# Kernel tuning notes

Measured on AMD Instinct MI355X. Metric: run time of the kernel, lower is better.

## Reference

```python
import jax, jax.numpy as jnp
import numpy as np

D_MODEL = 1024
NUM_HEADS = 16
D_HEAD = D_MODEL // NUM_HEADS
THETA = 10000.0


def setup_inputs() -> dict:
    key = jax.random.key(0)
    ks = jax.random.split(key, 5)
    B, S = 2, 2048
    std = np.sqrt(2.0 / (D_MODEL + D_MODEL))
    return {
        "x": jax.random.normal(ks[0], (B, S, D_MODEL), dtype=jnp.float32),
        "token_positions": jnp.arange(S, dtype=jnp.int32),
        "wq": jax.random.normal(ks[1], (D_MODEL, D_MODEL), dtype=jnp.float32) * std,
        "wk": jax.random.normal(ks[2], (D_MODEL, D_MODEL), dtype=jnp.float32) * std,
        "wv": jax.random.normal(ks[3], (D_MODEL, D_MODEL), dtype=jnp.float32) * std,
        "wo": jax.random.normal(ks[4], (D_MODEL, D_MODEL), dtype=jnp.float32) * std,
    }


def _rope(x, token_positions):
    # x: [B, H, S, D_HEAD]; token_positions: [S]
    freq_idx = jnp.arange(0, D_HEAD, 2, dtype=jnp.float32)
    inv_freq = THETA ** (-freq_idx / D_HEAD)                      # [D_HEAD/2]
    angles = token_positions.astype(jnp.float32)[:, None] * inv_freq  # [S, D_HEAD/2]
    cos = jnp.cos(angles)[None, None, :, :]
    sin = jnp.sin(angles)[None, None, :, :]
    x_even = x[..., 0::2]
    x_odd = x[..., 1::2]
    rot_even = x_even * cos - x_odd * sin
    rot_odd = x_even * sin + x_odd * cos
    # interleave pairs back: [..., pairs, 2] -> [..., D_HEAD]
    return jnp.stack((rot_even, rot_odd), axis=-1).reshape(x.shape)


def reference(x, token_positions, wq, wk, wv, wo):
    B, S, _ = x.shape
    def proj(w):
        y = jnp.einsum('bsi,oi->bso', x, w)
        return y.reshape(B, S, NUM_HEADS, D_HEAD).transpose(0, 2, 1, 3)  # [B,H,S,Dh]
    q = _rope(proj(wq), token_positions)
    k = _rope(proj(wk), token_positions)
    v = proj(wv)
    scores = jnp.einsum('bhqd,bhkd->bhqk', q, k) / jnp.sqrt(jnp.float32(D_HEAD))
    causal = jnp.tril(jnp.ones((S, S), dtype=bool))
    scores = jnp.where(causal, scores, -jnp.inf)
    probs = jax.nn.softmax(scores, axis=-1)
    attn = jnp.einsum('bhqk,bhkd->bhqd', probs, v)
    attn = attn.transpose(0, 2, 1, 3).reshape(B, S, D_MODEL)
    return jnp.einsum('bsi,oi->bso', attn, wo)
```

## Files before the change

kernel.cpp:

```cpp
#include <hip/hip_runtime.h>
#include <math.h>

#define D_MODEL 1024
#define NUM_HEADS 16
#define D_HEAD 64
#define SEQ 2048
#define BATCH 2

typedef __attribute__((ext_vector_type(8))) short short8;
typedef __attribute__((ext_vector_type(4))) short short4v;
typedef __attribute__((ext_vector_type(4))) float float4v;
typedef __attribute__((ext_vector_type(2))) unsigned int uint2v;

__device__ __forceinline__ short f2bf(float f) {
    unsigned u = __float_as_uint(f);
    u += 0x7FFFu + ((u >> 16) & 1u);
    return (short)(u >> 16);
}

__device__ __forceinline__ float fexp2(float x) {
    return __builtin_amdgcn_exp2f(x);
}

__global__ __launch_bounds__(256) void cvt_bf16_kernel(
    const float* __restrict__ x,  const float* __restrict__ wq,
    const float* __restrict__ wk, const float* __restrict__ wv,
    const float* __restrict__ wo, const int* __restrict__ pos,
    short* __restrict__ xb,  short* __restrict__ wqb,
    short* __restrict__ wkb, short* __restrict__ wvb,
    short* __restrict__ wob,
    float* __restrict__ costab, float* __restrict__ sintab)
{
    const int a = blockIdx.y;
    if (a == 5) {
        const int idx = blockIdx.x * 256 + threadIdx.x;
        if (idx < SEQ * 32) {
            const int s = idx >> 5, fi = idx & 31;
            const float p = (float)pos[s];
            const float inv_freq = exp2f((float)fi * -0.4152410118609203f);
            float sn, cs;
            sincosf(p * inv_freq, &sn, &cs);
            costab[idx] = cs;
            sintab[idx] = sn;
        }
        return;
    }
    const float* src = (a == 0) ? x : (a == 1) ? wq : (a == 2) ? wk : (a == 3) ? wv : wo;
    short* dst = (a == 0) ? xb : (a == 1) ? wqb : (a == 2) ? wkb : (a == 3) ? wvb : wob;
    const int n = (a == 0) ? (BATCH * SEQ * D_MODEL) : (D_MODEL * D_MODEL);
    const int i = (blockIdx.x * 256 + threadIdx.x) * 8;
    if (i >= n) return;
    const float4 v0 = *(const float4*)(src + i);
    const float4 v1 = *(const float4*)(src + i + 4);
    short8 r;
    r[0] = f2bf(v0.x); r[1] = f2bf(v0.y); r[2] = f2bf(v0.z); r[3] = f2bf(v0.w);
    r[4] = f2bf(v1.x); r[5] = f2bf(v1.y); r[6] = f2bf(v1.z); r[7] = f2bf(v1.w);
    *(short8*)(dst + i) = r;
}

__device__ __forceinline__ void gemm_core_db(
    const short* __restrict__ a, const short* __restrict__ b,
    short* smem, int m0, int n0, float4v acc[4][4], const int nk)
{
    const int tid = threadIdx.x;
    const int lane = tid & 63;
    const int l15 = lane & 15, quad = lane >> 4;
    const int wave = tid >> 6;
    const int mw = (wave & 1) * 64, nw = (wave >> 1) * 64;
    const int srow = tid >> 2;
    const int scol = (tid & 3) * 8;
    const int ssw = (((tid & 3) ^ ((srow >> 1) & 3))) * 8;
    const int xsw = (l15 >> 1) & 3;

    const short* ag = a + (size_t)(m0 + srow) * D_MODEL + scol;
    const short* bg = b + (size_t)(n0 + srow) * D_MODEL + scol;

    short* bufA[2] = { smem,        smem + 8192 };
    short* bufB[2] = { smem + 4096, smem + 12288 };

    short8 ga0 = *(const short8*)(ag);
    short8 ga1 = *(const short8*)(ag + (size_t)64 * D_MODEL);
    short8 gb0 = *(const short8*)(bg);
    short8 gb1 = *(const short8*)(bg + (size_t)64 * D_MODEL);
    *(short8*)&bufA[0][srow * 32 + ssw]        = ga0;
    *(short8*)&bufA[0][(64 + srow) * 32 + ssw] = ga1;
    *(short8*)&bufB[0][srow * 32 + ssw]        = gb0;
    *(short8*)&bufB[0][(64 + srow) * 32 + ssw] = gb1;
    ga0 = *(const short8*)(ag + 32);
    ga1 = *(const short8*)(ag + 32 + (size_t)64 * D_MODEL);
    gb0 = *(const short8*)(bg + 32);
    gb1 = *(const short8*)(bg + 32 + (size_t)64 * D_MODEL);

    for (int k = 0; k < nk; k++) {
        __syncthreads();
        if (k + 1 < nk) {
            short* bA = bufA[(k + 1) & 1];
            short* bB = bufB[(k + 1) & 1];
            *(short8*)&bA[srow * 32 + ssw]        = ga0;
            *(short8*)&bA[(64 + srow) * 32 + ssw] = ga1;
            *(short8*)&bB[srow * 32 + ssw]        = gb0;
            *(short8*)&bB[(64 + srow) * 32 + ssw] = gb1;
        }
        if (k + 2 < nk) {
            const int off = (k + 2) * 32;
            ga0 = *(const short8*)(ag + off);
            ga1 = *(const short8*)(ag + off + (size_t)64 * D_MODEL);
            gb0 = *(const short8*)(bg + off);
            gb1 = *(const short8*)(bg + off + (size_t)64 * D_MODEL);
        }
        const short* lA = bufA[k & 1];
        const short* lB = bufB[k & 1];
        short8 af[4], bf[4];
        #pragma unroll
        for (int i = 0; i < 4; i++)
            af[i] = *(const short8*)&lA[(mw + i * 16 + l15) * 32 + (quad ^ xsw) * 8];
        #pragma unroll
        for (int i = 0; i < 4; i++)
            bf[i] = *(const short8*)&lB[(nw + i * 16 + l15) * 32 + (quad ^ xsw) * 8];
        #pragma unroll
        for (int mi = 0; mi < 4; mi++)
            #pragma unroll
            for (int ni = 0; ni < 4; ni++)
                acc[mi][ni] = __builtin_amdgcn_mfma_f32_16x16x32_bf16(
                    af[mi], bf[ni], acc[mi][ni], 0, 0, 0);
    }
}

__device__ __forceinline__ void gemm_core_out(
    const short* __restrict__ a, const short* __restrict__ b,
    short* smem, int m0, int n0, float4v acc[2][4])
{
    const int tid = threadIdx.x;
    const int lane = tid & 63;
    const int l15 = lane & 15, quad = lane >> 4;
    const int wave = tid >> 6;
    const int mw = wave * 32;
    const int srow = tid >> 2;
    const int scol = (tid & 3) * 8;
    const int ssw = (((tid & 3) ^ ((srow >> 1) & 3))) * 8;
    const int xsw = (l15 >> 1) & 3;

    const short* ag = a + (size_t)(m0 + srow) * D_MODEL + scol;
    const short* bg = b + (size_t)(n0 + srow) * D_MODEL + scol;

    short* bufA[2] = { smem,        smem + 6144 };
    short* bufB[2] = { smem + 4096, smem + 10240 };

    short8 ga0 = *(const short8*)(ag);
    short8 ga1 = *(const short8*)(ag + (size_t)64 * D_MODEL);
    short8 gb0 = *(const short8*)(bg);
    *(short8*)&bufA[0][srow * 32 + ssw]        = ga0;
    *(short8*)&bufA[0][(64 + srow) * 32 + ssw] = ga1;
    *(short8*)&bufB[0][srow * 32 + ssw]        = gb0;
    ga0 = *(const short8*)(ag + 32);
    ga1 = *(const short8*)(ag + 32 + (size_t)64 * D_MODEL);
    gb0 = *(const short8*)(bg + 32);

    for (int k = 0; k < 32; k++) {
        __syncthreads();
        if (k + 1 < 32) {
            short* bA = bufA[(k + 1) & 1];
            short* bB = bufB[(k + 1) & 1];
            *(short8*)&bA[srow * 32 + ssw]        = ga0;
            *(short8*)&bA[(64 + srow) * 32 + ssw] = ga1;
            *(short8*)&bB[srow * 32 + ssw]        = gb0;
        }
        if (k + 2 < 32) {
            const int off = (k + 2) * 32;
            ga0 = *(const short8*)(ag + off);
            ga1 = *(const short8*)(ag + off + (size_t)64 * D_MODEL);
            gb0 = *(const short8*)(bg + off);
        }
        const short* lA = bufA[k & 1];
        const short* lB = bufB[k & 1];
        short8 af[2], bf[4];
        #pragma unroll
        for (int i = 0; i < 2; i++)
            af[i] = *(const short8*)&lA[(mw + i * 16 + l15) * 32 + (quad ^ xsw) * 8];
        #pragma unroll
        for (int i = 0; i < 4; i++)
            bf[i] = *(const short8*)&lB[(i * 16 + l15) * 32 + (quad ^ xsw) * 8];
        #pragma unroll
        for (int mi = 0; mi < 2; mi++)
            #pragma unroll
            for (int ni = 0; ni < 4; ni++)
                acc[mi][ni] = __builtin_amdgcn_mfma_f32_16x16x32_bf16(
                    af[mi], bf[ni], acc[mi][ni], 0, 0, 0);
    }
}

__global__ __launch_bounds__(256) void qkv_mfma_kernel(
    const short* __restrict__ xb, const short* __restrict__ wqb,
    const short* __restrict__ wkb, const short* __restrict__ wvb,
    const float* __restrict__ costab, const float* __restrict__ sintab,
    short* __restrict__ Qb, short* __restrict__ Kb, short* __restrict__ Vt)
{
    __shared__ __align__(16) short smem[128 * 136];

    const int z = blockIdx.x >> 8;
    const int bid = blockIdx.x & 255;
    const int m0 = (bid & 31) * 128;
    const int n0 = (bid >> 5) * 128;
    const short* w = (z == 0) ? wqb : (z == 1) ? wkb : wvb;

    float4v acc[4][4];
    #pragma unroll
    for (int i = 0; i < 4; i++)
        #pragma unroll
        for (int j = 0; j < 4; j++)
            acc[i][j] = (float4v){0.f, 0.f, 0.f, 0.f};

    gemm_core_db(xb, w, smem, m0, n0, acc, 32);

    const int tid = threadIdx.x;
    const int lane = tid & 63;
    const int l15 = lane & 15, quad = lane >> 4;
    const int wave = tid >> 6;
    const int mw = (wave & 1) * 64, nw = (wave >> 1) * 64;
    const int s_base = m0 & (SEQ - 1);
    const int bb = m0 >> 11;

    __syncthreads();

    if (z == 2) {
        #pragma unroll
        for (int ni = 0; ni < 4; ni++) {
            #pragma unroll
            for (int mi = 0; mi < 4; mi++) {
                #pragma unroll
                for (int r = 0; r < 4; r++)
                    smem[(nw + ni * 16 + l15) * 136 + mw + mi * 16 + quad * 4 + r] =
                        f2bf(acc[mi][ni][r]);
            }
        }
        __syncthreads();
        #pragma unroll
        for (int it = 0; it < 8; it++) {
            const int nloc = it * 16 + (tid >> 4);
            const int mloc = (tid & 15) * 8;
            const short8 val = *(const short8*)&smem[nloc * 136 + mloc];
            const int n = n0 + nloc;
            const int h = n >> 6, d = n & 63;
            *(short8*)(Vt + ((size_t)(bb * NUM_HEADS + h) * D_HEAD + d) * SEQ +
                       s_base + mloc) = val;
        }
    } else {
        short* dst = (z == 0) ? Qb : Kb;
        const float qs = (z == 0) ? 0.18033688011112042f : 1.0f;
        #pragma unroll
        for (int ni = 0; ni < 4; ni++) {
            const int n = n0 + nw + ni * 16 + l15;
            const int d = n & 63;
            const int fi = d >> 1;
            #pragma unroll
            for (int mi = 0; mi < 4; mi++) {
                #pragma unroll
                for (int r = 0; r < 4; r++) {
                    const int mloc = mw + mi * 16 + quad * 4 + r;
                    const int ti = ((s_base + mloc) << 5) + fi;
                    const float cs = costab[ti];
                    const float sn = sintab[ti];
                    const float val = acc[mi][ni][r];
                    const float partner = __shfl_xor(val, 1, 64);
                    const float res = (l15 & 1) ? fmaf(partner, sn, val * cs)
                                                : fmaf(val, cs, -partner * sn);
                    smem[mloc * 136 + nw + ni * 16 + l15] = f2bf(res * qs);
                }
            }
        }
        __syncthreads();
        #pragma unroll
        for (int it = 0; it < 8; it++) {
            const int ri = it * 32 + (tid >> 3);
            const int mloc = ri & 127;
            const int hh = ri >> 7;
            const int nloc = hh * 64 + (tid & 7) * 8;
            const short8 val = *(const short8*)&smem[mloc * 136 + nloc];
            const int n = n0 + nloc;
            const int h = n >> 6, d = n & 63;
            *(short8*)(dst + ((size_t)(bb * NUM_HEADS + h) * SEQ + s_base + mloc) *
                       D_HEAD + d) = val;
        }
    }
}

__global__ __launch_bounds__(256) void attn_mfma_kernel(
    const short* __restrict__ Qb, const short* __restrict__ Kb,
    const short* __restrict__ Vt, short* __restrict__ Ab)
{
    __shared__ __align__(16) short lKa[64 * 32];
    __shared__ __align__(16) short lKb[64 * 32];
    __shared__ __align__(16) short lVa[64 * 32];
    __shared__ __align__(16) short lVb[64 * 32];
    __shared__ __align__(16) short lP[4][2][16 * 32];

    const int tid = threadIdx.x;
    const int lane = tid & 63;
    const int wave = tid >> 6;
    const int l15 = lane & 15;
    const int quad = lane >> 4;

    const int bh = blockIdx.x & (BATCH * NUM_HEADS - 1);
    const int qt = (SEQ / 64 - 1) - (blockIdx.x >> 5);
    const int q0w = qt * 64 + wave * 16;
    const int qcmp = q0w + l15;

    const short* Kg = Kb + (size_t)bh * SEQ * D_HEAD;
    const short* Vg = Vt + (size_t)bh * D_HEAD * SEQ;

    const short* Qrow = Qb + ((size_t)bh * SEQ + q0w + l15) * D_HEAD;
    const short8 qf0 = *(const short8*)(Qrow + quad * 8);
    const short8 qf1 = *(const short8*)(Qrow + 32 + quad * 8);

    float4v o0 = {0.f, 0.f, 0.f, 0.f}, o1 = o0, o2 = o0, o3 = o0;
    float lpA = 0.f, lpB = 0.f;

    const int nt = qt + 1;
    const int srow = tid >> 2;
    const int c4  = tid & 3;
    const int sch = c4 * 8;
    const int swoff = srow * 32 + ((c4 ^ ((srow >> 1) & 3)) * 8);
    const int xsw = (l15 >> 1) & 3;

    short8 k0 = *(const short8*)(Kg + (size_t)srow * D_HEAD + sch);
    short8 k1 = *(const short8*)(Kg + (size_t)srow * D_HEAD + sch + 32);
    short8 v0 = *(const short8*)(Vg + (size_t)srow * SEQ + sch);
    short8 v1 = *(const short8*)(Vg + (size_t)srow * SEQ + sch + 32);

#define ATTN_TILE_COMPUTE(KT0, MASKED)                                        \
    {                                                                         \
        short* PwA = &lP[wave][0][0];                                         \
        short* PwB = &lP[wave][1][0];                                         \
        _Pragma("unroll")                                                     \
        for (int g = 0; g < 4; g++) {                                         \
            float4v s = {0.f, 0.f, 0.f, 0.f};                                 \
            const int krow = (g * 16 + l15) * 32 + (quad ^ xsw) * 8;          \
            const short8 ka = *(const short8*)&lKa[krow];                     \
            const short8 kb = *(const short8*)&lKb[krow];                     \
            __builtin_amdgcn_s_setprio(1);                                    \
            s = __builtin_amdgcn_mfma_f32_16x16x32_bf16(ka, qf0, s, 0, 0, 0); \
            s = __builtin_amdgcn_mfma_f32_16x16x32_bf16(kb, qf1, s, 0, 0, 0); \
            __builtin_amdgcn_s_setprio(0);                                    \
            float e0, e1, e2, e3;                                             \
            if (MASKED) {                                                     \
                const int kbase = (KT0) + g * 16 + quad * 4;                  \
                e0 = (kbase + 0 <= qcmp) ? fexp2(s[0]) : 0.f;                 \
                e1 = (kbase + 1 <= qcmp) ? fexp2(s[1]) : 0.f;                 \
                e2 = (kbase + 2 <= qcmp) ? fexp2(s[2]) : 0.f;                 \
                e3 = (kbase + 3 <= qcmp) ? fexp2(s[3]) : 0.f;                 \
            } else {                                                          \
                e0 = fexp2(s[0]); e1 = fexp2(s[1]);                           \
                e2 = fexp2(s[2]); e3 = fexp2(s[3]);                           \
            }                                                                 \
            lpA += e0 + e2;                                                   \
            lpB += e1 + e3;                                                   \
            unsigned int pw0, pw1;                                            \
            asm("v_cvt_pk_bf16_f32 %0, %1, %2" : "=v"(pw0) : "v"(e0), "v"(e1)); \
            asm("v_cvt_pk_bf16_f32 %0, %1, %2" : "=v"(pw1) : "v"(e2), "v"(e3)); \
            uint2v pk; pk[0] = pw0; pk[1] = pw1;                              \
            short* Pd = (g < 2) ? PwA : PwB;                                  \
            const int ps = ((((g & 1) * 2 + (quad >> 1)) ^ xsw) * 8) +        \
                           (quad & 1) * 4;                                    \
            *(uint2v*)&Pd[l15 * 32 + ps] = pk;                                \
        }                                                                     \
        const int prow = l15 * 32 + (quad ^ xsw) * 8;                         \
        const short8 pa0 = *(const short8*)&PwA[prow];                        \
        const short8 pa1 = *(const short8*)&PwB[prow];                        \
        __builtin_amdgcn_s_setprio(1);                                        \
        _Pragma("unroll")                                                     \
        for (int j = 0; j < 4; j++) {                                         \
            const int vrow = (j * 16 + l15) * 32 + (quad ^ xsw) * 8;          \
            const short8 va = *(const short8*)&lVa[vrow];                     \
            const short8 vb = *(const short8*)&lVb[vrow];                     \
            float4v* oj = (j == 0) ? &o0 : (j == 1) ? &o1 : (j == 2) ? &o2 : &o3;       \
            *oj = __builtin_amdgcn_mfma_f32_16x16x32_bf16(pa0, va, *oj, 0, 0, 0);       \
            *oj = __builtin_amdgcn_mfma_f32_16x16x32_bf16(pa1, vb, *oj, 0, 0, 0);       \
        }                                                                     \
        __builtin_amdgcn_s_setprio(0);                                        \
    }

    for (int t = 0; t < nt - 1; t++) {
        const int kt0 = t * 64;
        __syncthreads();
        *(short8*)&lKa[swoff] = k0;
        *(short8*)&lKb[swoff] = k1;
        *(short8*)&lVa[swoff] = v0;
        *(short8*)&lVb[swoff] = v1;
        __syncthreads();
        k0 = *(const short8*)(Kg + (size_t)(kt0 + 64 + srow) * D_HEAD + sch);
        k1 = *(const short8*)(Kg + (size_t)(kt0 + 64 + srow) * D_HEAD + sch + 32);
        v0 = *(const short8*)(Vg + (size_t)srow * SEQ + kt0 + 64 + sch);
        v1 = *(const short8*)(Vg + (size_t)srow * SEQ + kt0 + 64 + sch + 32);
        ATTN_TILE_COMPUTE(kt0, false)
    }
    {
        const int kt0 = (nt - 1) * 64;
        __syncthreads();
        *(short8*)&lKa[swoff] = k0;
        *(short8*)&lKb[swoff] = k1;
        *(short8*)&lVa[swoff] = v0;
        *(short8*)&lVb[swoff] = v1;
        __syncthreads();
        ATTN_TILE_COMPUTE(kt0, true)
    }
#undef ATTN_TILE_COMPUTE

    float lp = lpA + lpB;
    lp += __shfl_xor(lp, 16, 64);
    lp += __shfl_xor(lp, 32, 64);

    const int b = bh >> 4, h = bh & 15;
    short* Ap = Ab + ((size_t)(b * SEQ) + q0w + quad * 4) * D_MODEL + h * D_HEAD;
    #pragma unroll
    for (int r = 0; r < 4; r++) {
        const float inv = 1.0f / __shfl(lp, quad * 4 + r, 64);
        Ap[(size_t)r * D_MODEL + l15]      = f2bf(o0[r] * inv);
        Ap[(size_t)r * D_MODEL + 16 + l15] = f2bf(o1[r] * inv);
        Ap[(size_t)r * D_MODEL + 32 + l15] = f2bf(o2[r] * inv);
        Ap[(size_t)r * D_MODEL + 48 + l15] = f2bf(o3[r] * inv);
    }
}

__global__ __launch_bounds__(256) void out_mfma_kernel(
    const short* __restrict__ Ab, const short* __restrict__ wob,
    float* __restrict__ out)
{
    __shared__ __align__(16) short smem[12288];

    const int bid = blockIdx.x;
    const int m0 = (bid & 31) * 128;
    const int n0 = (bid >> 5) * 64;

    float4v acc[2][4];
    #pragma unroll
    for (int i = 0; i < 2; i++)
        #pragma unroll
        for (int j = 0; j < 4; j++)
            acc[i][j] = (float4v){0.f, 0.f, 0.f, 0.f};

    gemm_core_out(Ab, wob, smem, m0, n0, acc);

    const int tid = threadIdx.x;
    const int lane = tid & 63;
    const int l15 = lane & 15, quad = lane >> 4;
    const int wave = tid >> 6;
    const int mw = wave * 32;

    #pragma unroll
    for (int mi = 0; mi < 2; mi++) {
        #pragma unroll
        for (int r = 0; r < 4; r++) {
            const int m = m0 + mw + mi * 16 + quad * 4 + r;
            float* op = out + (size_t)m * D_MODEL + n0 + l15;
            #pragma unroll
            for (int ni = 0; ni < 4; ni++)
                op[ni * 16] = acc[mi][ni][r];
        }
    }
}

extern "C" void kernel_launch(void* const* d_in, const int* in_sizes, int n_in,
                              void* d_out, int out_size, void* d_ws, size_t ws_size,
                              hipStream_t stream)
{
    const float* x  = (const float*)d_in[0];
    const int*  pos = (const int*)d_in[1];
    const float* wq = (const float*)d_in[2];
    const float* wk = (const float*)d_in[3];
    const float* wv = (const float*)d_in[4];
    const float* wo = (const float*)d_in[5];
    float* out = (float*)d_out;

    const size_t nx = (size_t)BATCH * SEQ * D_MODEL;
    const size_t nw = (size_t)D_MODEL * D_MODEL;
    short* xb  = (short*)d_ws;
    short* wqb = xb + nx;
    short* wkb = wqb + nw;
    short* wvb = wkb + nw;
    short* wob = wvb + nw;
    short* Qb  = wob + nw;
    short* Kb  = Qb + nx;
    short* Vt  = Kb + nx;
    short* Ab  = Vt + nx;
    float* costab = (float*)(Ab + nx);
    float* sintab = costab + SEQ * 32;

    dim3 blk(256);
    cvt_bf16_kernel<<<dim3(2048, 6), blk, 0, stream>>>(x, wq, wk, wv, wo, pos,
                                                       xb, wqb, wkb, wvb, wob,
                                                       costab, sintab);
    qkv_mfma_kernel<<<dim3(768), blk, 0, stream>>>(xb, wqb, wkb, wvb,
                                                   costab, sintab, Qb, Kb, Vt);
    attn_mfma_kernel<<<dim3(BATCH * NUM_HEADS * (SEQ / 64)), blk, 0, stream>>>(Qb, Kb, Vt, Ab);
    out_mfma_kernel<<<dim3(512), blk, 0, stream>>>(Ab, wob, out);
}
```

Before: 174.7 us.

## Fuse fp32-to-bf16 conversion into GEMM loaders and compute RoPE inline

Removes the separate conversion kernel. The QKV and output GEMMs now load fp32 inputs and weights directly and convert them to bf16 with packed cvt instructions while staging into shared memory. RoPE sin and cos are computed in the epilogue with hardware sin/cos on fractional revolutions instead of reading precomputed tables. This saves one launch and the bf16 round-trip through global memory, at the cost of twice the global bytes per GEMM tile load, redundant conversion of x across the column blocks, and lower-precision hardware trig.

Measured after the change: 208.2 us. 1.19x slower.

```diff
diff --git a/kernel.cpp b/kernel.cpp
--- a/kernel.cpp
+++ b/kernel.cpp
@@ -8,9 +8,9 @@
 #define BATCH 2
 
 typedef __attribute__((ext_vector_type(8))) short short8;
-typedef __attribute__((ext_vector_type(4))) short short4v;
 typedef __attribute__((ext_vector_type(4))) float float4v;
 typedef __attribute__((ext_vector_type(2))) unsigned int uint2v;
+typedef __attribute__((ext_vector_type(4))) unsigned int uint4v;
 
 __device__ __forceinline__ short f2bf(float f) {
     unsigned u = __float_as_uint(f);
@@ -22,45 +22,25 @@
     return __builtin_amdgcn_exp2f(x);
 }
 
-__global__ __launch_bounds__(256) void cvt_bf16_kernel(
-    const float* __restrict__ x,  const float* __restrict__ wq,
-    const float* __restrict__ wk, const float* __restrict__ wv,
-    const float* __restrict__ wo, const int* __restrict__ pos,
-    short* __restrict__ xb,  short* __restrict__ wqb,
-    short* __restrict__ wkb, short* __restrict__ wvb,
-    short* __restrict__ wob,
-    float* __restrict__ costab, float* __restrict__ sintab)
-{
-    const int a = blockIdx.y;
-    if (a == 5) {
-        const int idx = blockIdx.x * 256 + threadIdx.x;
-        if (idx < SEQ * 32) {
-            const int s = idx >> 5, fi = idx & 31;
-            const float p = (float)pos[s];
-            const float inv_freq = exp2f((float)fi * -0.4152410118609203f);
-            float sn, cs;
-            sincosf(p * inv_freq, &sn, &cs);
-            costab[idx] = cs;
-            sintab[idx] = sn;
-        }
-        return;
-    }
-    const float* src = (a == 0) ? x : (a == 1) ? wq : (a == 2) ? wk : (a == 3) ? wv : wo;
-    short* dst = (a == 0) ? xb : (a == 1) ? wqb : (a == 2) ? wkb : (a == 3) ? wvb : wob;
-    const int n = (a == 0) ? (BATCH * SEQ * D_MODEL) : (D_MODEL * D_MODEL);
-    const int i = (blockIdx.x * 256 + threadIdx.x) * 8;
-    if (i >= n) return;
-    const float4 v0 = *(const float4*)(src + i);
-    const float4 v1 = *(const float4*)(src + i + 4);
-    short8 r;
-    r[0] = f2bf(v0.x); r[1] = f2bf(v0.y); r[2] = f2bf(v0.z); r[3] = f2bf(v0.w);
-    r[4] = f2bf(v1.x); r[5] = f2bf(v1.y); r[6] = f2bf(v1.z); r[7] = f2bf(v1.w);
-    *(short8*)(dst + i) = r;
-}
-
-__device__ __forceinline__ void gemm_core_db(
-    const short* __restrict__ a, const short* __restrict__ b,
-    short* smem, int m0, int n0, float4v acc[4][4], const int nk)
+__device__ __forceinline__ uint4v cvt8(float4 lo, float4 hi) {
+    uint4v r;
+    asm("v_cvt_pk_bf16_f32 %0, %1, %2" : "=v"(r[0]) : "v"(lo.x), "v"(lo.y));
+    asm("v_cvt_pk_bf16_f32 %0, %1, %2" : "=v"(r[1]) : "v"(lo.z), "v"(lo.w));
+    asm("v_cvt_pk_bf16_f32 %0, %1, %2" : "=v"(r[2]) : "v"(hi.x), "v"(hi.y));
+    asm("v_cvt_pk_bf16_f32 %0, %1, %2" : "=v"(r[3]) : "v"(hi.z), "v"(hi.w));
+    return r;
+}
+
+__device__ __forceinline__ void sincos_rev(float rev, float* sn, float* cs) {
+    float fr;
+    asm("v_fract_f32 %0, %1" : "=v"(fr) : "v"(rev));
+    asm("v_sin_f32 %0, %1" : "=v"(*sn) : "v"(fr));
+    asm("v_cos_f32 %0, %1" : "=v"(*cs) : "v"(fr));
+}
+
+__device__ __forceinline__ void gemm_core_f32(
+    const float* __restrict__ a, const float* __restrict__ b,
+    short* smem, int m0, int n0, float4v acc[4][4])
 {
     const int tid = threadIdx.x;
     const int lane = tid & 63;
@@ -72,41 +52,53 @@
     const int ssw = (((tid & 3) ^ ((srow >> 1) & 3))) * 8;
     const int xsw = (l15 >> 1) & 3;
 
-    const short* ag = a + (size_t)(m0 + srow) * D_MODEL + scol;
-    const short* bg = b + (size_t)(n0 + srow) * D_MODEL + scol;
+    const float* ag = a + (size_t)(m0 + srow) * D_MODEL + scol;
+    const float* bg = b + (size_t)(n0 + srow) * D_MODEL + scol;
 
     short* bufA[2] = { smem,        smem + 8192 };
     short* bufB[2] = { smem + 4096, smem + 12288 };
 
-    short8 ga0 = *(const short8*)(ag);
-    short8 ga1 = *(const short8*)(ag + (size_t)64 * D_MODEL);
-    short8 gb0 = *(const short8*)(bg);
-    short8 gb1 = *(const short8*)(bg + (size_t)64 * D_MODEL);
-    *(short8*)&bufA[0][srow * 32 + ssw]        = ga0;
-    *(short8*)&bufA[0][(64 + srow) * 32 + ssw] = ga1;
-    *(short8*)&bufB[0][srow * 32 + ssw]        = gb0;
-    *(short8*)&bufB[0][(64 + srow) * 32 + ssw] = gb1;
-    ga0 = *(const short8*)(ag + 32);
-    ga1 = *(const short8*)(ag + 32 + (size_t)64 * D_MODEL);
-    gb0 = *(const short8*)(bg + 32);
-    gb1 = *(const short8*)(bg + 32 + (size_t)64 * D_MODEL);
-
-    for (int k = 0; k < nk; k++) {
-        __syncthreads();
-        if (k + 1 < nk) {
+    float4 a0l = *(const float4*)(ag);
+    float4 a0h = *(const float4*)(ag + 4);
+    float4 a1l = *(const float4*)(ag + (size_t)64 * D_MODEL);
+    float4 a1h = *(const float4*)(ag + (size_t)64 * D_MODEL + 4);
+    float4 b0l = *(const float4*)(bg);
+    float4 b0h = *(const float4*)(bg + 4);
+    float4 b1l = *(const float4*)(bg + (size_t)64 * D_MODEL);
+    float4 b1h = *(const float4*)(bg + (size_t)64 * D_MODEL + 4);
+    *(uint4v*)&bufA[0][srow * 32 + ssw]        = cvt8(a0l, a0h);
+    *(uint4v*)&bufA[0][(64 + srow) * 32 + ssw] = cvt8(a1l, a1h);
+    *(uint4v*)&bufB[0][srow * 32 + ssw]        = cvt8(b0l, b0h);
+    *(uint4v*)&bufB[0][(64 + srow) * 32 + ssw] = cvt8(b1l, b1h);
+    a0l = *(const float4*)(ag + 32);
+    a0h = *(const float4*)(ag + 36);
+    a1l = *(const float4*)(ag + 32 + (size_t)64 * D_MODEL);
+    a1h = *(const float4*)(ag + 36 + (size_t)64 * D_MODEL);
+    b0l = *(const float4*)(bg + 32);
+    b0h = *(const float4*)(bg + 36);
+    b1l = *(const float4*)(bg + 32 + (size_t)64 * D_MODEL);
+    b1h = *(const float4*)(bg + 36 + (size_t)64 * D_MODEL);
+
+    for (int k = 0; k < 32; k++) {
+        __syncthreads();
+        if (k + 1 < 32) {
             short* bA = bufA[(k + 1) & 1];
             short* bB = bufB[(k + 1) & 1];
-            *(short8*)&bA[srow * 32 + ssw]        = ga0;
-            *(short8*)&bA[(64 + srow) * 32 + ssw] = ga1;
-            *(short8*)&bB[srow * 32 + ssw]        = gb0;
-            *(short8*)&bB[(64 + srow) * 32 + ssw] = gb1;
-        }
-        if (k + 2 < nk) {
+            *(uint4v*)&bA[srow * 32 + ssw]        = cvt8(a0l, a0h);
+            *(uint4v*)&bA[(64 + srow) * 32 + ssw] = cvt8(a1l, a1h);
+            *(uint4v*)&bB[srow * 32 + ssw]        = cvt8(b0l, b0h);
+            *(uint4v*)&bB[(64 + srow) * 32 + ssw] = cvt8(b1l, b1h);
+        }
+        if (k + 2 < 32) {
             const int off = (k + 2) * 32;
-            ga0 = *(const short8*)(ag + off);
-            ga1 = *(const short8*)(ag + off + (size_t)64 * D_MODEL);
-            gb0 = *(const short8*)(bg + off);
-            gb1 = *(const short8*)(bg + off + (size_t)64 * D_MODEL);
+            a0l = *(const float4*)(ag + off);
+            a0h = *(const float4*)(ag + off + 4);
+            a1l = *(const float4*)(ag + off + (size_t)64 * D_MODEL);
+            a1h = *(const float4*)(ag + off + 4 + (size_t)64 * D_MODEL);
+            b0l = *(const float4*)(bg + off);
+            b0h = *(const float4*)(bg + off + 4);
+            b1l = *(const float4*)(bg + off + (size_t)64 * D_MODEL);
+            b1h = *(const float4*)(bg + off + 4 + (size_t)64 * D_MODEL);
         }
         const short* lA = bufA[k & 1];
         const short* lB = bufB[k & 1];
@@ -127,7 +119,7 @@
 }
 
 __device__ __forceinline__ void gemm_core_out(
-    const short* __restrict__ a, const short* __restrict__ b,
+    const short* __restrict__ a, const float* __restrict__ b,
     short* smem, int m0, int n0, float4v acc[2][4])
 {
     const int tid = threadIdx.x;
@@ -141,20 +133,22 @@
     const int xsw = (l15 >> 1) & 3;
 
     const short* ag = a + (size_t)(m0 + srow) * D_MODEL + scol;
-    const short* bg = b + (size_t)(n0 + srow) * D_MODEL + scol;
+    const float* bg = b + (size_t)(n0 + srow) * D_MODEL + scol;
 
     short* bufA[2] = { smem,        smem + 6144 };
     short* bufB[2] = { smem + 4096, smem + 10240 };
 
     short8 ga0 = *(const short8*)(ag);
     short8 ga1 = *(const short8*)(ag + (size_t)64 * D_MODEL);
-    short8 gb0 = *(const short8*)(bg);
+    float4 b0l = *(const float4*)(bg);
+    float4 b0h = *(const float4*)(bg + 4);
     *(short8*)&bufA[0][srow * 32 + ssw]        = ga0;
     *(short8*)&bufA[0][(64 + srow) * 32 + ssw] = ga1;
-    *(short8*)&bufB[0][srow * 32 + ssw]        = gb0;
+    *(uint4v*)&bufB[0][srow * 32 + ssw]        = cvt8(b0l, b0h);
     ga0 = *(const short8*)(ag + 32);
     ga1 = *(const short8*)(ag + 32 + (size_t)64 * D_MODEL);
-    gb0 = *(const short8*)(bg + 32);
+    b0l = *(const float4*)(bg + 32);
+    b0h = *(const float4*)(bg + 36);
 
     for (int k = 0; k < 32; k++) {
         __syncthreads();
@@ -163,13 +157,14 @@
             short* bB = bufB[(k + 1) & 1];
             *(short8*)&bA[srow * 32 + ssw]        = ga0;
             *(short8*)&bA[(64 + srow) * 32 + ssw] = ga1;
-            *(short8*)&bB[srow * 32 + ssw]        = gb0;
+            *(uint4v*)&bB[srow * 32 + ssw]        = cvt8(b0l, b0h);
         }
         if (k + 2 < 32) {
             const int off = (k + 2) * 32;
             ga0 = *(const short8*)(ag + off);
             ga1 = *(const short8*)(ag + off + (size_t)64 * D_MODEL);
-            gb0 = *(const short8*)(bg + off);
+            b0l = *(const float4*)(bg + off);
+            b0h = *(const float4*)(bg + off + 4);
         }
         const short* lA = bufA[k & 1];
         const short* lB = bufB[k & 1];
@@ -190,9 +185,9 @@
 }
 
 __global__ __launch_bounds__(256) void qkv_mfma_kernel(
-    const short* __restrict__ xb, const short* __restrict__ wqb,
-    const short* __restrict__ wkb, const short* __restrict__ wvb,
-    const float* __restrict__ costab, const float* __restrict__ sintab,
+    const float* __restrict__ x, const float* __restrict__ wq,
+    const float* __restrict__ wk, const float* __restrict__ wv,
+    const int* __restrict__ pos,
     short* __restrict__ Qb, short* __restrict__ Kb, short* __restrict__ Vt)
 {
     __shared__ __align__(16) short smem[128 * 136];
@@ -201,7 +196,7 @@
     const int bid = blockIdx.x & 255;
     const int m0 = (bid & 31) * 128;
     const int n0 = (bid >> 5) * 128;
-    const short* w = (z == 0) ? wqb : (z == 1) ? wkb : wvb;
+    const float* w = (z == 0) ? wq : (z == 1) ? wk : wv;
 
     float4v acc[4][4];
     #pragma unroll
@@ -210,7 +205,7 @@
         for (int j = 0; j < 4; j++)
             acc[i][j] = (float4v){0.f, 0.f, 0.f, 0.f};
 
-    gemm_core_db(xb, w, smem, m0, n0, acc, 32);
+    gemm_core_f32(x, w, smem, m0, n0, acc);
 
     const int tid = threadIdx.x;
     const int lane = tid & 63;
@@ -247,19 +242,28 @@
     } else {
         short* dst = (z == 0) ? Qb : Kb;
         const float qs = (z == 0) ? 0.18033688011112042f : 1.0f;
+
+        float pf[4][4];
+        #pragma unroll
+        for (int mi = 0; mi < 4; mi++)
+            #pragma unroll
+            for (int r = 0; r < 4; r++)
+                pf[mi][r] = (float)pos[s_base + mw + mi * 16 + quad * 4 + r];
+
         #pragma unroll
         for (int ni = 0; ni < 4; ni++) {
             const int n = n0 + nw + ni * 16 + l15;
             const int d = n & 63;
             const int fi = d >> 1;
+            const float invrev = fexp2((float)fi * -0.4152410118609203f) *
+                                 0.15915494309189535f;
             #pragma unroll
             for (int mi = 0; mi < 4; mi++) {
                 #pragma unroll
                 for (int r = 0; r < 4; r++) {
                     const int mloc = mw + mi * 16 + quad * 4 + r;
-                    const int ti = ((s_base + mloc) << 5) + fi;
-                    const float cs = costab[ti];
-                    const float sn = sintab[ti];
+                    float sn, cs;
+                    sincos_rev(pf[mi][r] * invrev, &sn, &cs);
                     const float val = acc[mi][ni][r];
                     const float partner = __shfl_xor(val, 1, 64);
                     const float res = (l15 & 1) ? fmaf(partner, sn, val * cs)
@@ -422,7 +426,7 @@
 }
 
 __global__ __launch_bounds__(256) void out_mfma_kernel(
-    const short* __restrict__ Ab, const short* __restrict__ wob,
+    const short* __restrict__ Ab, const float* __restrict__ wo,
     float* __restrict__ out)
 {
     __shared__ __align__(16) short smem[12288];
@@ -438,7 +442,7 @@
         for (int j = 0; j < 4; j++)
             acc[i][j] = (float4v){0.f, 0.f, 0.f, 0.f};
 
-    gemm_core_out(Ab, wob, smem, m0, n0, acc);
+    gemm_core_out(Ab, wo, smem, m0, n0, acc);
 
     const int tid = threadIdx.x;
     const int lane = tid & 63;
@@ -472,25 +476,14 @@
     float* out = (float*)d_out;
 
     const size_t nx = (size_t)BATCH * SEQ * D_MODEL;
-    const size_t nw = (size_t)D_MODEL * D_MODEL;
-    short* xb  = (short*)d_ws;
-    short* wqb = xb + nx;
-    short* wkb = wqb + nw;
-    short* wvb = wkb + nw;
-    short* wob = wvb + nw;
-    short* Qb  = wob + nw;
+    short* Qb  = (short*)d_ws;
     short* Kb  = Qb + nx;
     short* Vt  = Kb + nx;
     short* Ab  = Vt + nx;
-    float* costab = (float*)(Ab + nx);
-    float* sintab = costab + SEQ * 32;
 
     dim3 blk(256);
-    cvt_bf16_kernel<<<dim3(2048, 6), blk, 0, stream>>>(x, wq, wk, wv, wo, pos,
-                                                       xb, wqb, wkb, wvb, wob,
-                                                       costab, sintab);
-    qkv_mfma_kernel<<<dim3(768), blk, 0, stream>>>(xb, wqb, wkb, wvb,
-                                                   costab, sintab, Qb, Kb, Vt);
+    qkv_mfma_kernel<<<dim3(768), blk, 0, stream>>>(x, wq, wk, wv, pos,
+                                                   Qb, Kb, Vt);
     attn_mfma_kernel<<<dim3(BATCH * NUM_HEADS * (SEQ / 64)), blk, 0, stream>>>(Qb, Kb, Vt, Ab);
-    out_mfma_kernel<<<dim3(512), blk, 0, stream>>>(Ab, wob, out);
-}
+    out_mfma_kernel<<<dim3(512), blk, 0, stream>>>(Ab, wo, out);
+}
```
